# Optimization experiments

Hardware: AMD Instinct MI355X
Metric: run time of the kernel (lower is better)

Reference implementation:

```python
import jax, jax.numpy as jnp
import numpy as np

N_NODES = 100000
N_EDGES = 1000000
D_IN = 64
FEATURES = [64, 64, 16]


def setup_inputs() -> dict:
    key = jax.random.key(0)
    ks = jax.random.split(key, 10)
    nodes = jax.random.normal(ks[0], (N_NODES, D_IN), dtype=jnp.float32)
    senders = jax.random.randint(ks[1], (N_EDGES,), 0, N_NODES, dtype=jnp.int64)
    receivers = jax.random.randint(ks[2], (N_EDGES,), 0, N_NODES, dtype=jnp.int64)
    dims = [D_IN] + FEATURES
    params = {}
    for i in range(len(FEATURES)):
        fan_in = dims[i]
        # hk.Linear default: truncated-normal-ish init; plain normal scaled is fine for a reference
        params[f"W{i}"] = jax.random.normal(ks[3 + i], (dims[i], dims[i + 1]), dtype=jnp.float32) / np.sqrt(fan_in)
        params[f"b{i}"] = jnp.zeros((dims[i + 1],), dtype=jnp.float32)
    return {"nodes": nodes, "senders": senders, "receivers": receivers, **params}


def _gcn_layer(h, senders, receivers, W, b, use_tanh, add_self_edges):
    N = h.shape[0]
    h = h @ W + b
    if use_tanh:
        h = jnp.tanh(h)
    if add_self_edges:
        self_idx = jnp.arange(N, dtype=senders.dtype)
        s = jnp.concatenate([senders, self_idx], axis=0)
        r = jnp.concatenate([receivers, self_idx], axis=0)
    else:
        s, r = senders, receivers
    ones = jnp.ones(s.shape, dtype=h.dtype)
    deg_s = jax.ops.segment_sum(ones, s, num_segments=N)
    deg_r = jax.ops.segment_sum(ones, r, num_segments=N)
    h = h * jax.lax.rsqrt(jnp.maximum(deg_s, 1.0))[:, None]
    h = jax.ops.segment_sum(h[s], r, num_segments=N)  # gather -> scatter-add
    h = h * jax.lax.rsqrt(jnp.maximum(deg_r, 1.0))[:, None]
    return h


def reference(nodes, senders, receivers, W0, b0, W1, b1, W2, b2):
    h = nodes
    # layers over features[:-1]: tanh activation, self edges added
    h = _gcn_layer(h, senders, receivers, W0, b0, use_tanh=True, add_self_edges=True)
    h = _gcn_layer(h, senders, receivers, W1, b1, use_tanh=True, add_self_edges=True)
    # final layer: linear only, no self edges, still symmetric normalization
    h = _gcn_layer(h, senders, receivers, W2, b2, use_tanh=False, add_self_edges=False)
    return h
```

## Files before the change

### kernel.cpp

```cpp
#include <hip/hip_runtime.h>


#define CAP 32
#define BSH 7
#define BW 128
#define BCAP 1664
#define EPT 4

typedef unsigned short u16;
typedef unsigned int u32;

__device__ __forceinline__ float bf2f(u16 u) {
    return __uint_as_float(((u32)u) << 16);
}
__device__ __forceinline__ u16 f2bf(float f) {
    u32 x = __float_as_uint(f);
    u32 r = x + 0x7fff + ((x >> 16) & 1);
    return (u16)(r >> 16);
}
__device__ __forceinline__ float fast_tanh(float x) {
    x = fminf(15.f, fmaxf(-15.f, x));
    float e = __expf(2.f * x);
    return (e - 1.f) / (e + 1.f);
}
__device__ __forceinline__ int unpack_deg(const u32* pk, int n) {
    return (int)((pk[n >> 2] >> (8 * (n & 3))) & 255u);
}

__global__ __launch_bounds__(256) void k_init(int* __restrict__ curR,
                                              int* __restrict__ curS, int nbuk) {
    int t = blockIdx.x * 256 + threadIdx.x;
    if (t < nbuk) {
        curR[t] = t * BCAP;
        curS[t] = t * BCAP;
    }
}

__global__ __launch_bounds__(1024) void k_part(const int* __restrict__ s,
                                               const int* __restrict__ r,
                                               int* __restrict__ curR,
                                               int* __restrict__ curS,
                                               int2* __restrict__ pairR,
                                               int* __restrict__ svalS,
                                               int E, int nbuk) {
    __shared__ int cR[1024], cS[1024], bR[1024], bS[1024];
    const int t = threadIdx.x;
    for (int i = t; i < nbuk; i += 1024) { cR[i] = 0; cS[i] = 0; }
    __syncthreads();

    int ss[EPT], rr[EPT];
    const int base = blockIdx.x * (1024 * EPT);
#pragma unroll
    for (int i = 0; i < EPT; ++i) {
        int e = base + i * 1024 + t;
        ss[i] = (e < E) ? s[e] : -1;
        rr[i] = (e < E) ? r[e] : -1;
    }
#pragma unroll
    for (int i = 0; i < EPT; ++i) {
        if (rr[i] >= 0) {
            atomicAdd(&cR[rr[i] >> BSH], 1);
            atomicAdd(&cS[ss[i] >> BSH], 1);
        }
    }
    __syncthreads();
    for (int i = t; i < nbuk; i += 1024) {
        bR[i] = cR[i] ? atomicAdd(&curR[i], cR[i]) : 0;
        bS[i] = cS[i] ? atomicAdd(&curS[i], cS[i]) : 0;
    }
    __syncthreads();
    for (int i = t; i < nbuk; i += 1024) { cR[i] = 0; cS[i] = 0; }
    __syncthreads();
#pragma unroll
    for (int i = 0; i < EPT; ++i) {
        if (rr[i] >= 0) {
            int rb = rr[i] >> BSH;
            int pos = bR[rb] + atomicAdd(&cR[rb], 1);
            if (pos < (rb + 1) * BCAP) pairR[pos] = make_int2(ss[i], rr[i]);
            int sb = ss[i] >> BSH;
            int ps = bS[sb] + atomicAdd(&cS[sb], 1);
            if (ps < (sb + 1) * BCAP) svalS[ps] = ss[i];
        }
    }
}

__global__ __launch_bounds__(256) void k_ellb(const int2* __restrict__ pairR,
                                              const int* __restrict__ curR,
                                              int* __restrict__ ell,
                                              u32* __restrict__ degIp) {
    __shared__ int degLoc[BW];
    const int b = blockIdx.x, t = threadIdx.x;
    if (t < BW) degLoc[t] = 0;
    __syncthreads();
    const int start = b * BCAP;
    const int cnt = min(curR[b] - start, BCAP);
    for (int e = t; e < cnt; e += 256) {
        int2 p = pairR[start + e];
        int slot = atomicAdd(&degLoc[p.y - (b << BSH)], 1);
        if (slot < CAP) ell[p.y * CAP + slot] = p.x;
    }
    __syncthreads();
    if (t < BW / 4) {
        u32 w = (u32)min(degLoc[4 * t], 255) |
                ((u32)min(degLoc[4 * t + 1], 255) << 8) |
                ((u32)min(degLoc[4 * t + 2], 255) << 16) |
                ((u32)min(degLoc[4 * t + 3], 255) << 24);
        degIp[(b << (BSH - 2)) + t] = w;
    }
}

__global__ __launch_bounds__(256) void k_dego(const int* __restrict__ svalS,
                                              const int* __restrict__ curS,
                                              u32* __restrict__ degOp) {
    __shared__ int degLoc[BW];
    const int b = blockIdx.x, t = threadIdx.x;
    if (t < BW) degLoc[t] = 0;
    __syncthreads();
    const int start = b * BCAP;
    const int cnt = min(curS[b] - start, BCAP);
    for (int e = t; e < cnt; e += 256) {
        atomicAdd(&degLoc[svalS[start + e] - (b << BSH)], 1);
    }
    __syncthreads();
    if (t < BW / 4) {
        u32 w = (u32)min(degLoc[4 * t], 255) |
                ((u32)min(degLoc[4 * t + 1], 255) << 8) |
                ((u32)min(degLoc[4 * t + 2], 255) << 16) |
                ((u32)min(degLoc[4 * t + 3], 255) << 24);
        degOp[(b << (BSH - 2)) + t] = w;
    }
}

__global__ __launch_bounds__(256, 4) void k_transform64(const float* __restrict__ in,
                                                        const float* __restrict__ W,
                                                        const float* __restrict__ b,
                                                        const u32* __restrict__ degOp,
                                                        u16* __restrict__ out, int N) {
    __shared__ float4 lds[4][128];
    const int lane = threadIdx.x & 63;
    const int wv = threadIdx.x >> 6;

    float wc[64];
#pragma unroll
    for (int k = 0; k < 64; ++k) wc[k] = W[k * 64 + lane];
    const float bias = b[lane];

    const int base = blockIdx.x * 32 + wv * 8;
    const float4* in4 = (const float4*)in;
#pragma unroll
    for (int r2 = 0; r2 < 2; ++r2) {
        int idx = r2 * 64 + lane;
        int nn = base + (idx >> 4);
        float4 v = {0.f, 0.f, 0.f, 0.f};
        if (nn < N) v = in4[(size_t)base * 16 + idx];
        lds[wv][idx] = v;
    }
#pragma unroll
    for (int i = 0; i < 8; ++i) {
        const int n = base + i;
        if (n >= N) break;
        float acc = 0.f;
#pragma unroll
        for (int kk = 0; kk < 16; ++kk) {
            float4 h = lds[wv][i * 16 + kk];
            acc = fmaf(h.x, wc[4 * kk + 0], acc);
            acc = fmaf(h.y, wc[4 * kk + 1], acc);
            acc = fmaf(h.z, wc[4 * kk + 2], acc);
            acc = fmaf(h.w, wc[4 * kk + 3], acc);
        }
        float as01 = rsqrtf((float)unpack_deg(degOp, n) + 1.f);
        acc = fast_tanh(acc + bias) * as01;
        out[(size_t)n * 64 + lane] = f2bf(acc);
    }
}

__global__ __launch_bounds__(256, 4) void k_fgt64(const u16* __restrict__ h,
                                                  const u32* __restrict__ degOp,
                                                  const u32* __restrict__ degIp,
                                                  const int* __restrict__ ell,
                                                  const float* __restrict__ W,
                                                  const float* __restrict__ b,
                                                  u16* __restrict__ y, int N) {
    const int lane = threadIdx.x & 63;
    const int wv = __builtin_amdgcn_readfirstlane(threadIdx.x >> 6);

    float wc[64];
#pragma unroll
    for (int k = 0; k < 64; ++k) wc[k] = W[k * 64 + lane];
    const float bias = b[lane];

    const int base = blockIdx.x * 32 + wv * 8;
    for (int i8 = 0; i8 < 8; ++i8) {
        const int n = base + i8;
        if (n >= N) break;
        const int di = unpack_deg(degIp, n);
        const int deg = min(di, CAP);
        const int ng = (deg + 7) >> 3;
        const int* __restrict__ rowp = ell + (size_t)n * CAP;

        u16 aself = h[(size_t)n * 64 + lane];

        u16 a[32];
#pragma unroll
        for (int gi = 0; gi < 4; ++gi) {
            if (gi < ng) {
#pragma unroll
                for (int j = 0; j < 8; ++j) {
                    int e = gi * 8 + j;
                    int id = (e < deg) ? rowp[e] : n;
                    a[e] = h[(size_t)id * 64 + lane];
                }
            }
        }

        float acc = 0.f;
#pragma unroll
        for (int gi = 0; gi < 4; ++gi) {
            if (gi < ng) {
#pragma unroll
                for (int j = 0; j < 8; ++j) {
                    int e = gi * 8 + j;
                    acc += (e < deg) ? bf2f(a[e]) : 0.f;
                }
            }
        }
        acc += bf2f(aself);

        const float inscale = rsqrtf((float)di + 1.f);
        const float outscale = rsqrtf((float)unpack_deg(degOp, n) + 1.f);

        float d0 = 0.f, d1 = 0.f, d2 = 0.f, d3 = 0.f;
#pragma unroll
        for (int k = 0; k < 16; ++k) {
            d0 = fmaf(__uint_as_float(__builtin_amdgcn_readlane(
                     __float_as_uint(acc), k)),      wc[k],      d0);
            d1 = fmaf(__uint_as_float(__builtin_amdgcn_readlane(
                     __float_as_uint(acc), k + 16)), wc[k + 16], d1);
            d2 = fmaf(__uint_as_float(__builtin_amdgcn_readlane(
                     __float_as_uint(acc), k + 32)), wc[k + 32], d2);
            d3 = fmaf(__uint_as_float(__builtin_amdgcn_readlane(
                     __float_as_uint(acc), k + 48)), wc[k + 48], d3);
        }
        float dot = (d0 + d1) + (d2 + d3);
        float v = fast_tanh(fmaf(dot, inscale, bias)) * outscale;
        y[(size_t)n * 64 + lane] = f2bf(v);
    }
}

__global__ __launch_bounds__(256, 4) void k_fgt16(const u16* __restrict__ h,
                                                  const u32* __restrict__ degOp,
                                                  const u32* __restrict__ degIp,
                                                  const int* __restrict__ ell,
                                                  const float* __restrict__ W,
                                                  const float* __restrict__ b,
                                                  u16* __restrict__ y16, int N) {
    __shared__ float4 lds[4][16];
    const int lane = threadIdx.x & 63;
    const int wv = threadIdx.x >> 6;
    const int g = lane >> 4, c = lane & 15;
    const int j = lane & 15;

    float wc[16];
#pragma unroll
    for (int kk = 0; kk < 16; ++kk) wc[kk] = W[(16 * g + kk) * 16 + j];
    const float bias = b[j];

    const ushort4* h4 = (const ushort4*)h;
    const int base = blockIdx.x * 32 + wv * 8;
    for (int i8 = 0; i8 < 8; ++i8) {
        const int n = base + i8;
        if (n >= N) break;
        const int di = unpack_deg(degIp, n);
        const int deg = min(di, CAP);
        int idxv = (lane < CAP) ? ell[n * CAP + lane] : 0;

        float4 acc = {0.f, 0.f, 0.f, 0.f};
        const int jn = (deg + 3) >> 2;
        for (int jj = 0; jj < jn; ++jj) {
            int i = g + 4 * jj;
            int id = __shfl(idxv, i, 64);
            if (i < deg) {
                ushort4 v = h4[(size_t)id * 16 + c];
                acc.x += bf2f(v.x); acc.y += bf2f(v.y);
                acc.z += bf2f(v.z); acc.w += bf2f(v.w);
            }
        }
#pragma unroll
        for (int m = 16; m <= 32; m <<= 1) {
            acc.x += __shfl_xor(acc.x, m, 64);
            acc.y += __shfl_xor(acc.y, m, 64);
            acc.z += __shfl_xor(acc.z, m, 64);
            acc.w += __shfl_xor(acc.w, m, 64);
        }
        ushort4 sv = h4[(size_t)n * 16 + c];
        acc.x += bf2f(sv.x); acc.y += bf2f(sv.y);
        acc.z += bf2f(sv.z); acc.w += bf2f(sv.w);
        if (g == 0) lds[wv][c] = acc;

        const float* row = (const float*)lds[wv];
        float dot = 0.f;
#pragma unroll
        for (int kk = 0; kk < 16; ++kk) dot = fmaf(row[16 * g + kk], wc[kk], dot);
#pragma unroll
        for (int m = 16; m <= 32; m <<= 1) dot += __shfl_xor(dot, m, 64);

        if (g == 0) {
            const float inscale = rsqrtf((float)di + 1.f);
            const float outscale = rsqrtf(fmaxf((float)unpack_deg(degOp, n), 1.f));
            float v = fmaf(dot, inscale, bias) * outscale;
            y16[(size_t)n * 16 + j] = f2bf(v);
        }
    }
}

__global__ __launch_bounds__(256) void k_g16(const u16* __restrict__ h,
                                             const u32* __restrict__ degIp,
                                             const int* __restrict__ ell,
                                             float* __restrict__ out, int N) {
    const int lane = threadIdx.x & 63;
    const int wv = threadIdx.x >> 6;
    const int n = blockIdx.x * 4 + wv;
    if (n >= N) return;
    const int g = lane >> 2, c = lane & 3;
    const int di = unpack_deg(degIp, n);
    const int deg = min(di, CAP);
    int idxv = (lane < CAP) ? ell[n * CAP + lane] : 0;

    const ushort4* h4 = (const ushort4*)h;
    float4 acc = {0.f, 0.f, 0.f, 0.f};
    const int jn = (deg + 15) >> 4;
    for (int j = 0; j < jn; ++j) {
        int i = g + 16 * j;
        int id = __shfl(idxv, i, 64);
        if (i < deg) {
            ushort4 v = h4[(size_t)id * 4 + c];
            acc.x += bf2f(v.x); acc.y += bf2f(v.y);
            acc.z += bf2f(v.z); acc.w += bf2f(v.w);
        }
    }
#pragma unroll
    for (int m = 4; m <= 32; m <<= 1) {
        acc.x += __shfl_xor(acc.x, m, 64);
        acc.y += __shfl_xor(acc.y, m, 64);
        acc.z += __shfl_xor(acc.z, m, 64);
        acc.w += __shfl_xor(acc.w, m, 64);
    }
    if (g == 0) {
        float sc = rsqrtf(fmaxf((float)di, 1.f));
        acc.x *= sc; acc.y *= sc; acc.z *= sc; acc.w *= sc;
        ((float4*)out)[(size_t)n * 4 + c] = acc;
    }
}

extern "C" void kernel_launch(void* const* d_in, const int* in_sizes, int n_in,
                              void* d_out, int out_size, void* d_ws, size_t ws_size,
                              hipStream_t stream) {
    const float* nodes = (const float*)d_in[0];
    const int* senders = (const int*)d_in[1];
    const int* receivers = (const int*)d_in[2];
    const float* W0 = (const float*)d_in[3];
    const float* b0 = (const float*)d_in[4];
    const float* W1 = (const float*)d_in[5];
    const float* b1 = (const float*)d_in[6];
    const float* W2 = (const float*)d_in[7];
    const float* b2 = (const float*)d_in[8];
    float* out = (float*)d_out;

    const int N = in_sizes[0] / 64;
    const int E = in_sizes[1];
    const int nbuk = (N + BW - 1) >> BSH;
    const int nwords = nbuk * (BW / 4);

    u16* A = (u16*)d_ws;
    u16* B = A + (size_t)N * 64;
    u16* Y16 = B + (size_t)N * 64;
    u32* degOp = (u32*)(Y16 + (size_t)N * 16);
    u32* degIp = degOp + nwords;
    int* curR = (int*)(degIp + nwords);
    int* curS = curR + nbuk;
    int* ell = (int*)(curS + nbuk);
    int2* pairR = (int2*)(ell + (size_t)N * CAP);
    int* svalS = (int*)(pairR + (size_t)nbuk * BCAP);

    k_init<<<(nbuk + 255) / 256, 256, 0, stream>>>(curR, curS, nbuk);
    const int pblk = (E + 1024 * EPT - 1) / (1024 * EPT);
    k_part<<<pblk, 1024, 0, stream>>>(senders, receivers, curR, curS,
                                      pairR, svalS, E, nbuk);
    k_ellb<<<nbuk, 256, 0, stream>>>(pairR, curR, ell, degIp);
    k_dego<<<nbuk, 256, 0, stream>>>(svalS, curS, degOp);

    const int tb = (N + 31) / 32;
    const int fb = (N + 31) / 32;
    const int gb = (N + 3) / 4;

    k_transform64<<<tb, 256, 0, stream>>>(nodes, W0, b0, degOp, A, N);
    k_fgt64<<<fb, 256, 0, stream>>>(A, degOp, degIp, ell, W1, b1, B, N);
    k_fgt16<<<fb, 256, 0, stream>>>(B, degOp, degIp, ell, W2, b2, Y16, N);
    k_g16<<<gb, 256, 0, stream>>>(Y16, degIp, ell, out, N);
}
```

Baseline: 273.2 us.

## Split layer-2 fused gather-transform into separate gather and dense kernels

Replaces the fused gather+matmul+tanh kernel for the second layer with two kernels. The first gathers neighbour rows into an fp32 buffer without holding weight registers, which allows higher occupancy for latency-bound gathers. The second applies the 64x64 transform using readlane broadcasts. This costs an extra fp32 round trip of N*64 through memory and an extra launch, and it only runs when the workspace is large enough.

```diff
diff --git a/kernel.cpp b/kernel.cpp
--- a/kernel.cpp
+++ b/kernel.cpp
@@ -171,6 +171,83 @@
         float as01 = rsqrtf((float)unpack_deg(degOp, n) + 1.f);
         acc = fast_tanh(acc + bias) * as01;
         out[(size_t)n * 64 + lane] = f2bf(acc);
+    }
+}
+
+__global__ __launch_bounds__(256) void k_gath64(const u16* __restrict__ h,
+                                                const u32* __restrict__ degIp,
+                                                const int* __restrict__ ell,
+                                                float* __restrict__ G, int N) {
+    const int lane = threadIdx.x & 63;
+    const int wv = __builtin_amdgcn_readfirstlane(threadIdx.x >> 6);
+
+    const int base = blockIdx.x * 16 + wv * 4;
+#pragma unroll
+    for (int i4 = 0; i4 < 4; ++i4) {
+        const int n = base + i4;
+        if (n >= N) break;
+        const int di = unpack_deg(degIp, n);
+        const int deg = min(di, CAP);
+        const int* __restrict__ rowp = ell + (size_t)n * CAP;
+
+        u16 aself = h[(size_t)n * 64 + lane];
+        u16 a[16];
+#pragma unroll
+        for (int e = 0; e < 16; ++e) {
+            int id = (e < deg) ? rowp[e] : n;
+            a[e] = h[(size_t)id * 64 + lane];
+        }
+        float acc = 0.f;
+#pragma unroll
+        for (int e = 0; e < 16; ++e) acc += (e < deg) ? bf2f(a[e]) : 0.f;
+        for (int e = 16; e < deg; ++e) {
+            int id = rowp[e];
+            acc += bf2f(h[(size_t)id * 64 + lane]);
+        }
+        acc += bf2f(aself);
+        G[(size_t)n * 64 + lane] = acc;
+    }
+}
+
+__global__ __launch_bounds__(256, 4) void k_dense64(const float* __restrict__ G,
+                                                    const u32* __restrict__ degOp,
+                                                    const u32* __restrict__ degIp,
+                                                    const float* __restrict__ W,
+                                                    const float* __restrict__ b,
+                                                    u16* __restrict__ y, int N) {
+    const int lane = threadIdx.x & 63;
+    const int wv = __builtin_amdgcn_readfirstlane(threadIdx.x >> 6);
+
+    float wc[64];
+#pragma unroll
+    for (int k = 0; k < 64; ++k) wc[k] = W[k * 64 + lane];
+    const float bias = b[lane];
+
+    const int base = blockIdx.x * 32 + wv * 8;
+    for (int i8 = 0; i8 < 8; ++i8) {
+        const int n = base + i8;
+        if (n >= N) break;
+        const int di = unpack_deg(degIp, n);
+        const float inscale = rsqrtf((float)di + 1.f);
+        const float outscale = rsqrtf((float)unpack_deg(degOp, n) + 1.f);
+
+        const float acc = G[(size_t)n * 64 + lane];
+
+        float d0 = 0.f, d1 = 0.f, d2 = 0.f, d3 = 0.f;
+#pragma unroll
+        for (int k = 0; k < 16; ++k) {
+            d0 = fmaf(__uint_as_float(__builtin_amdgcn_readlane(
+                     __float_as_uint(acc), k)),      wc[k],      d0);
+            d1 = fmaf(__uint_as_float(__builtin_amdgcn_readlane(
+                     __float_as_uint(acc), k + 16)), wc[k + 16], d1);
+            d2 = fmaf(__uint_as_float(__builtin_amdgcn_readlane(
+                     __float_as_uint(acc), k + 32)), wc[k + 32], d2);
+            d3 = fmaf(__uint_as_float(__builtin_amdgcn_readlane(
+                     __float_as_uint(acc), k + 48)), wc[k + 48], d3);
+        }
+        float dot = (d0 + d1) + (d2 + d3);
+        float v = fast_tanh(fmaf(dot, inscale, bias)) * outscale;
+        y[(size_t)n * 64 + lane] = f2bf(v);
     }
 }
 
@@ -381,6 +458,9 @@
     int* ell = (int*)(curS + nbuk);
     int2* pairR = (int2*)(ell + (size_t)N * CAP);
     int* svalS = (int*)(pairR + (size_t)nbuk * BCAP);
+    float* G = (float*)(svalS + (size_t)nbuk * BCAP);
+    const size_t need = (size_t)((char*)(G + (size_t)N * 64) - (char*)d_ws);
+    const bool use_split = (ws_size >= need);
 
     k_init<<<(nbuk + 255) / 256, 256, 0, stream>>>(curR, curS, nbuk);
     const int pblk = (E + 1024 * EPT - 1) / (1024 * EPT);
@@ -391,10 +471,16 @@
 
     const int tb = (N + 31) / 32;
     const int fb = (N + 31) / 32;
+    const int gatb = (N + 15) / 16;
     const int gb = (N + 3) / 4;
 
     k_transform64<<<tb, 256, 0, stream>>>(nodes, W0, b0, degOp, A, N);
-    k_fgt64<<<fb, 256, 0, stream>>>(A, degOp, degIp, ell, W1, b1, B, N);
+    if (use_split) {
+        k_gath64<<<gatb, 256, 0, stream>>>(A, degIp, ell, G, N);
+        k_dense64<<<fb, 256, 0, stream>>>(G, degOp, degIp, W1, b1, B, N);
+    } else {
+        k_fgt64<<<fb, 256, 0, stream>>>(A, degOp, degIp, ell, W1, b1, B, N);
+    }
     k_fgt16<<<fb, 256, 0, stream>>>(B, degOp, degIp, ell, W2, b2, Y16, N);
     k_g16<<<gb, 256, 0, stream>>>(Y16, degIp, ell, out, N);
 }
```

Measured after the change: 282.6 us. 1.03x slower.

## Replace ELL gather layer with bucketed edge-pair scatter into LDS accumulators

Applied to the files above, without the earlier changes.

The second GCN layer no longer gathers neighbours through the per-node ELL table. Each block takes a bucket of 128 receiver nodes, walks that bucket's partitioned (sender, receiver) edge pairs, and atomically adds the gathered bf16 features into a 128x64 float LDS accumulator. The accumulated rows plus the self term are then multiplied by W1, with tanh and degree scaling applied in-block. This removes the CAP truncation and wasted padded gathers, at the cost of LDS float atomics, 32 KB of LDS per block limiting occupancy, and fewer, larger blocks.

```diff
diff --git a/kernel.cpp b/kernel.cpp
--- a/kernel.cpp
+++ b/kernel.cpp
@@ -174,74 +174,102 @@
     }
 }
 
-__global__ __launch_bounds__(256, 4) void k_fgt64(const u16* __restrict__ h,
-                                                  const u32* __restrict__ degOp,
-                                                  const u32* __restrict__ degIp,
-                                                  const int* __restrict__ ell,
-                                                  const float* __restrict__ W,
-                                                  const float* __restrict__ b,
-                                                  u16* __restrict__ y, int N) {
-    const int lane = threadIdx.x & 63;
-    const int wv = __builtin_amdgcn_readfirstlane(threadIdx.x >> 6);
+__global__ __launch_bounds__(256) void k_scat64(const u16* __restrict__ h,
+                                                const int2* __restrict__ pairR,
+                                                const int* __restrict__ curR,
+                                                const u32* __restrict__ degOp,
+                                                const u32* __restrict__ degIp,
+                                                const float* __restrict__ W,
+                                                const float* __restrict__ b,
+                                                u16* __restrict__ y, int N) {
+    __shared__ float acc[BW][64];
+    const int b_ = blockIdx.x, t = threadIdx.x;
+    const int lane = t & 63;
+    const int wv = t >> 6;
+    const int nb0 = b_ << BSH;
+
+    for (int i = t; i < BW * 64; i += 256) ((float*)acc)[i] = 0.f;
+    __syncthreads();
+
+    const int start = b_ * BCAP;
+    const int cnt = min(curR[b_] - start, BCAP);
+    const int ws = (cnt * wv) >> 2;
+    const int we = (cnt * (wv + 1)) >> 2;
+    int e = ws;
+    for (; e + 3 < we; e += 4) {
+        int2 p0 = pairR[start + e + 0];
+        int2 p1 = pairR[start + e + 1];
+        int2 p2 = pairR[start + e + 2];
+        int2 p3 = pairR[start + e + 3];
+        float v0 = bf2f(h[(size_t)p0.x * 64 + lane]);
+        float v1 = bf2f(h[(size_t)p1.x * 64 + lane]);
+        float v2 = bf2f(h[(size_t)p2.x * 64 + lane]);
+        float v3 = bf2f(h[(size_t)p3.x * 64 + lane]);
+        atomicAdd(&acc[p0.y - nb0][lane], v0);
+        atomicAdd(&acc[p1.y - nb0][lane], v1);
+        atomicAdd(&acc[p2.y - nb0][lane], v2);
+        atomicAdd(&acc[p3.y - nb0][lane], v3);
+    }
+    for (; e < we; ++e) {
+        int2 p = pairR[start + e];
+        float v = bf2f(h[(size_t)p.x * 64 + lane]);
+        atomicAdd(&acc[p.y - nb0][lane], v);
+    }
+    __syncthreads();
 
     float wc[64];
 #pragma unroll
     for (int k = 0; k < 64; ++k) wc[k] = W[k * 64 + lane];
     const float bias = b[lane];
 
-    const int base = blockIdx.x * 32 + wv * 8;
-    for (int i8 = 0; i8 < 8; ++i8) {
-        const int n = base + i8;
+    const ushort4* h4 = (const ushort4*)h;
+    for (int i = 0; i < 32; ++i) {
+        const int rl = wv * 32 + i;
+        const int n = nb0 + rl;
         if (n >= N) break;
+        const float4* row4 = (const float4*)acc[rl];
+        float d0 = 0.f, d1 = 0.f, d2 = 0.f, d3 = 0.f;
+#pragma unroll
+        for (int kk = 0; kk < 4; ++kk) {
+            float4 g = row4[kk];
+            ushort4 s4 = h4[(size_t)n * 16 + kk];
+            d0 = fmaf(g.x + bf2f(s4.x), wc[4 * kk + 0], d0);
+            d0 = fmaf(g.y + bf2f(s4.y), wc[4 * kk + 1], d0);
+            d0 = fmaf(g.z + bf2f(s4.z), wc[4 * kk + 2], d0);
+            d0 = fmaf(g.w + bf2f(s4.w), wc[4 * kk + 3], d0);
+        }
+#pragma unroll
+        for (int kk = 4; kk < 8; ++kk) {
+            float4 g = row4[kk];
+            ushort4 s4 = h4[(size_t)n * 16 + kk];
+            d1 = fmaf(g.x + bf2f(s4.x), wc[4 * kk + 0], d1);
+            d1 = fmaf(g.y + bf2f(s4.y), wc[4 * kk + 1], d1);
+            d1 = fmaf(g.z + bf2f(s4.z), wc[4 * kk + 2], d1);
+            d1 = fmaf(g.w + bf2f(s4.w), wc[4 * kk + 3], d1);
+        }
+#pragma unroll
+        for (int kk = 8; kk < 12; ++kk) {
+            float4 g = row4[kk];
+            ushort4 s4 = h4[(size_t)n * 16 + kk];
+            d2 = fmaf(g.x + bf2f(s4.x), wc[4 * kk + 0], d2);
+            d2 = fmaf(g.y + bf2f(s4.y), wc[4 * kk + 1], d2);
+            d2 = fmaf(g.z + bf2f(s4.z), wc[4 * kk + 2], d2);
+            d2 = fmaf(g.w + bf2f(s4.w), wc[4 * kk + 3], d2);
+        }
+#pragma unroll
+        for (int kk = 12; kk < 16; ++kk) {
+            float4 g = row4[kk];
+            ushort4 s4 = h4[(size_t)n * 16 + kk];
+            d3 = fmaf(g.x + bf2f(s4.x), wc[4 * kk + 0], d3);
+            d3 = fmaf(g.y + bf2f(s4.y), wc[4 * kk + 1], d3);
+            d3 = fmaf(g.z + bf2f(s4.z), wc[4 * kk + 2], d3);
+            d3 = fmaf(g.w + bf2f(s4.w), wc[4 * kk + 3], d3);
+        }
+        float dot = (d0 + d1) + (d2 + d3);
+
         const int di = unpack_deg(degIp, n);
-        const int deg = min(di, CAP);
-        const int ng = (deg + 7) >> 3;
-        const int* __restrict__ rowp = ell + (size_t)n * CAP;
-
-        u16 aself = h[(size_t)n * 64 + lane];
-
-        u16 a[32];
-#pragma unroll
-        for (int gi = 0; gi < 4; ++gi) {
-            if (gi < ng) {
-#pragma unroll
-                for (int j = 0; j < 8; ++j) {
-                    int e = gi * 8 + j;
-                    int id = (e < deg) ? rowp[e] : n;
-                    a[e] = h[(size_t)id * 64 + lane];
-                }
-            }
-        }
-
-        float acc = 0.f;
-#pragma unroll
-        for (int gi = 0; gi < 4; ++gi) {
-            if (gi < ng) {
-#pragma unroll
-                for (int j = 0; j < 8; ++j) {
-                    int e = gi * 8 + j;
-                    acc += (e < deg) ? bf2f(a[e]) : 0.f;
-                }
-            }
-        }
-        acc += bf2f(aself);
-
         const float inscale = rsqrtf((float)di + 1.f);
         const float outscale = rsqrtf((float)unpack_deg(degOp, n) + 1.f);
-
-        float d0 = 0.f, d1 = 0.f, d2 = 0.f, d3 = 0.f;
-#pragma unroll
-        for (int k = 0; k < 16; ++k) {
-            d0 = fmaf(__uint_as_float(__builtin_amdgcn_readlane(
-                     __float_as_uint(acc), k)),      wc[k],      d0);
-            d1 = fmaf(__uint_as_float(__builtin_amdgcn_readlane(
-                     __float_as_uint(acc), k + 16)), wc[k + 16], d1);
-            d2 = fmaf(__uint_as_float(__builtin_amdgcn_readlane(
-                     __float_as_uint(acc), k + 32)), wc[k + 32], d2);
-            d3 = fmaf(__uint_as_float(__builtin_amdgcn_readlane(
-                     __float_as_uint(acc), k + 48)), wc[k + 48], d3);
-        }
-        float dot = (d0 + d1) + (d2 + d3);
         float v = fast_tanh(fmaf(dot, inscale, bias)) * outscale;
         y[(size_t)n * 64 + lane] = f2bf(v);
     }
@@ -394,7 +422,8 @@
     const int gb = (N + 3) / 4;
 
     k_transform64<<<tb, 256, 0, stream>>>(nodes, W0, b0, degOp, A, N);
-    k_fgt64<<<fb, 256, 0, stream>>>(A, degOp, degIp, ell, W1, b1, B, N);
+    k_scat64<<<nbuk, 256, 0, stream>>>(A, pairR, curR, degOp, degIp,
+                                       W1, b1, B, N);
     k_fgt16<<<fb, 256, 0, stream>>>(B, degOp, degIp, ell, W2, b2, Y16, N);
     k_g16<<<gb, 256, 0, stream>>>(Y16, degIp, ell, out, N);
 }
```

After: 703.1 us. +157.4%, slower.
